# Performance work log

Hardware: AMD Instinct MI355X
Metric: run time of the kernel (lower is better)

The kernel has to match this reference:

```python
import jax, jax.numpy as jnp
import numpy as np

B, S, C, D, V = 64, 128, 32, 512, 20000

def setup_inputs() -> dict:
    key = jax.random.key(0)
    ks = jax.random.split(key, 16)
    sc = 1.0 / np.sqrt(D)
    emb = jax.random.normal(ks[0], (V + 1, D), jnp.float32) * 0.02
    emb = emb.at[V].set(0.0)  # padding_idx=-1 -> last row zero
    inp = dict(
        emb=emb,
        W_all_w=jax.random.uniform(ks[1], (4 * D, D), jnp.float32, -sc, sc),
        W_all_b=jnp.zeros((4 * D,), jnp.float32),
        U_all_w=jax.random.uniform(ks[2], (4 * D, D), jnp.float32, -sc, sc),
        U_all_b=jnp.zeros((4 * D,), jnp.float32),
        W_d_w=jax.random.uniform(ks[3], (D, D), jnp.float32, -sc, sc),
        W_d_b=jnp.zeros((D,), jnp.float32),
        sel_w=jax.random.uniform(ks[4], (64, 1), jnp.float32, -1.0, 1.0),
        sel_b=jnp.zeros((64,), jnp.float32),
        time_w=jax.random.uniform(ks[5], (D, 64), jnp.float32, -0.125, 0.125),
        time_b=jnp.zeros((D,), jnp.float32),
        out_w=jax.random.uniform(ks[6], (2, D), jnp.float32, -sc, sc),
        out_b=jnp.zeros((2,), jnp.float32),
        seq_time_step=jax.random.uniform(ks[7], (B, S), jnp.float32, 0.0, 365.0),
        input_seqs=jax.random.randint(ks[8], (B, S, C), 0, V),
        mask=jnp.zeros((B, S), bool),
        lengths=jax.random.randint(ks[9], (B,), 1, S),
        codemask=jnp.zeros((B, S, C), bool),
        label=jax.random.randint(ks[10], (B,), 0, 2),
    )
    return inp


def reference(emb, W_all_w, W_all_b, U_all_w, U_all_b, W_d_w, W_d_b,
              sel_w, sel_b, time_w, time_b, out_w, out_b, seq_time_step,
              input_seqs, mask, lengths, codemask, label):
    # visit embedding: sum code embeddings -> [B,S,D]
    x = emb[input_seqs].sum(axis=2)
    # time feature: 1 - tanh(selection_layer(t/180)^2) -> time_layer -> [B,S,D]
    t = (seq_time_step / 180.0)[..., None]                      # [B,S,1]
    tf = 1.0 - jnp.tanh(jnp.square(t * sel_w[:, 0] + sel_b))    # [B,S,64]
    tf = jnp.einsum('bsk,dk->bsd', tf, time_w) + time_b         # [B,S,D]
    # precompute input projection for all steps: [B,S,4D]
    ux = jnp.einsum('bsd,ed->bse', x, U_all_w) + U_all_b

    def step(carry, inputs):
        h, c = carry
        tf_s, ux_s = inputs                                      # [B,D], [B,4D]
        c_s1 = jnp.tanh(c @ W_d_w.T + W_d_b)
        c_adj = c - c_s1 + c_s1 * tf_s
        outs = h @ W_all_w.T + W_all_b + ux_s
        f, i, o, c_tmp = jnp.split(jax.nn.sigmoid(outs), 4, axis=1)
        c_new = f * c_adj + i * c_tmp
        h_new = o * jnp.tanh(c_new)
        return (h_new, c_new), h_new

    h0 = jnp.zeros((B, D), x.dtype)
    c0 = jnp.zeros((B, D), x.dtype)
    tf_t = jnp.swapaxes(tf, 0, 1)   # [S,B,D]
    ux_t = jnp.swapaxes(ux, 0, 1)   # [S,B,4D]
    _, hs = jax.lax.scan(step, (h0, c0), (tf_t, ux_t))
    outputs = jnp.swapaxes(hs, 0, 1)           # [B,S,D]
    pooled = outputs.max(axis=1)                # MaxPoolLayer without mask
    out = pooled @ out_w.T + out_b              # [B,2]
    return out
```

## Files before the change

### kernel.cpp

```cpp
#include <hip/hip_runtime.h>
#include <hip/hip_bf16.h>

#define B_ 64
#define S_ 128
#define C_ 32
#define D_ 512
#define V_ 20000

typedef float     f32x4  __attribute__((ext_vector_type(4)));
typedef _Float16  f16x8  __attribute__((ext_vector_type(8)));

#define OFF_XH   0ull
#define OFF_UH   8388608ull
#define OFF_AW   10485760ull
#define OFF_CB   13631488ull
#define OFF_SYNC 13639680ull
#define OFF_TWT  13647872ull
#define OFF_EMBH 13778944ull
#define OFF_TF   34259968ull
#define OFF_UX   42648576ull
#define OFF_XB2  76203008ull

#define SENT32 0x7FFF7FFFu

__global__ void k_zero(int4* __restrict__ p)
{
    p[blockIdx.x * 256 + threadIdx.x] = int4{0, 0, 0, 0};
}

__global__ void k_fill(int4* __restrict__ p)
{
    p[blockIdx.x * 256 + threadIdx.x] =
        int4{(int)SENT32, (int)SENT32, (int)SENT32, (int)SENT32};
}

__global__ void k_prep_wswz(const float* __restrict__ Wall, const float* __restrict__ Wd,
                            int4* __restrict__ AW)
{
    int i = blockIdx.x * 256 + threadIdx.x;
    int lane = i & 63;  int r = i >> 6;
    int kt = r & 15;    r >>= 4;
    int tile = r % 3;   r /= 3;
    int w = r & 7;      int m = r >> 3;
    int row16 = lane & 15, quad = lane >> 4;
    int q = tile * 2 + (row16 >> 3);
    int d = m * 64 + w * 8 + (row16 & 7);
    int k0 = kt * 32 + quad * 8;
    union { _Float16 h[8]; int4 v; } u;
    const float* src = nullptr;
    if (q < 4)       src = Wall + (size_t)(q * 512 + d) * 512 + k0;
    else if (q == 4) src = Wd   + (size_t)d * 512 + k0;
    #pragma unroll
    for (int j = 0; j < 8; j++) u.h[j] = src ? (_Float16)src[j] : (_Float16)0.f;
    AW[i] = u.v;
}

__global__ void k_prep_u(const float* __restrict__ U, _Float16* __restrict__ o)
{
    int i = blockIdx.x * 256 + threadIdx.x;
    o[i] = (_Float16)U[i];
}

__global__ void k_prep_cb(const float* __restrict__ a, const float* __restrict__ b,
                          float* __restrict__ o)
{
    int i = blockIdx.x * 256 + threadIdx.x;
    o[i] = a[i] + b[i];
}

__global__ void k_prep_emb(const float* __restrict__ e, _Float16* __restrict__ o)
{
    int i = blockIdx.x * 256 + threadIdx.x;
    float2 v = ((const float2*)e)[i];
    unsigned short hx = __builtin_bit_cast(unsigned short, (_Float16)v.x);
    unsigned short hy = __builtin_bit_cast(unsigned short, (_Float16)v.y);
    ((unsigned*)o)[i] = (unsigned)hx | ((unsigned)hy << 16);
}

__global__ void k_prep_twt(const float* __restrict__ tw, float* __restrict__ o)
{
    int i = blockIdx.x * 256 + threadIdx.x;
    int d = i >> 6, j = i & 63;
    o[j * 512 + d] = tw[i];
}

__global__ void k_embed2(const _Float16* __restrict__ embh, const int* __restrict__ seqs,
                         _Float16* __restrict__ xh)
{
    int bs = blockIdx.x;
    int t  = threadIdx.x;
    __shared__ int rows[32];
    if (t < 32) {
        int r = seqs[(size_t)bs * C_ + t];
        rows[t] = (r < 0) ? V_ : r;
    }
    __syncthreads();
    float ax = 0.f, ay = 0.f;
    #pragma unroll 4
    for (int c = 0; c < C_; c++) {
        unsigned v = *(const unsigned*)(embh + (size_t)rows[c] * D_ + 2 * t);
        ax += (float)__builtin_bit_cast(_Float16, (unsigned short)v);
        ay += (float)__builtin_bit_cast(_Float16, (unsigned short)(v >> 16));
    }
    unsigned short hx = __builtin_bit_cast(unsigned short, (_Float16)ax);
    unsigned short hy = __builtin_bit_cast(unsigned short, (_Float16)ay);
    *(unsigned*)(xh + (size_t)bs * D_ + 2 * t) = (unsigned)hx | ((unsigned)hy << 16);
}

__global__ __launch_bounds__(512) void k_tf2(
    const float* __restrict__ stime, const float* __restrict__ selw,
    const float* __restrict__ selb, const float* __restrict__ twT,
    const float* __restrict__ timeb, _Float16* __restrict__ tf)
{
    int bb = blockIdx.x;
    int t  = threadIdx.x;
    __shared__ float s1[16][64];
    for (int idx = t; idx < 1024; idx += 512) {
        int bl = idx >> 6, j = idx & 63;
        float tv = stime[bb * 16 + bl] * (1.0f / 180.0f);
        float u  = tv * selw[j] + selb[j];
        s1[bl][j] = 1.0f - tanhf(u * u);
    }
    __syncthreads();
    int d = t;
    float acc[16];
    float tb = timeb[d];
    #pragma unroll
    for (int l = 0; l < 16; l++) acc[l] = tb;
    for (int j = 0; j < 64; j++) {
        float wj = twT[j * 512 + d];
        #pragma unroll
        for (int l = 0; l < 16; l++) acc[l] = fmaf(s1[l][j], wj, acc[l]);
    }
    #pragma unroll
    for (int l = 0; l < 16; l++)
        tf[(size_t)(bb * 16 + l) * 512 + d] = (_Float16)acc[l];
}

__global__ __launch_bounds__(512) void k_gemm(const _Float16* __restrict__ A,
                                              const _Float16* __restrict__ Bm,
                                              _Float16* __restrict__ Cg)
{
    int lane = threadIdx.x & 63;
    int w    = threadIdx.x >> 6;
    int wm = w & 3, wn = w >> 2;
    int q = lane >> 4, r = lane & 15;
    int m0 = blockIdx.y * 128 + wm * 32;
    int n0 = blockIdx.x * 128 + wn * 64;

    const _Float16* pa0 = A  + (size_t)(m0 + r) * 512 + q * 8;
    const _Float16* pa1 = pa0 + (size_t)16 * 512;
    const _Float16* pb  = Bm + (size_t)(n0 + r) * 512 + q * 8;

    f32x4 acc[2][4] = {};
    for (int k = 0; k < 512; k += 32) {
        f16x8 a0 = *(const f16x8*)(pa0 + k);
        f16x8 a1 = *(const f16x8*)(pa1 + k);
        f16x8 b0 = *(const f16x8*)(pb + k);
        f16x8 b1 = *(const f16x8*)(pb + (size_t)16 * 512 + k);
        f16x8 b2 = *(const f16x8*)(pb + (size_t)32 * 512 + k);
        f16x8 b3 = *(const f16x8*)(pb + (size_t)48 * 512 + k);
        acc[0][0] = __builtin_amdgcn_mfma_f32_16x16x32_f16(a0, b0, acc[0][0], 0, 0, 0);
        acc[0][1] = __builtin_amdgcn_mfma_f32_16x16x32_f16(a0, b1, acc[0][1], 0, 0, 0);
        acc[0][2] = __builtin_amdgcn_mfma_f32_16x16x32_f16(a0, b2, acc[0][2], 0, 0, 0);
        acc[0][3] = __builtin_amdgcn_mfma_f32_16x16x32_f16(a0, b3, acc[0][3], 0, 0, 0);
        acc[1][0] = __builtin_amdgcn_mfma_f32_16x16x32_f16(a1, b0, acc[1][0], 0, 0, 0);
        acc[1][1] = __builtin_amdgcn_mfma_f32_16x16x32_f16(a1, b1, acc[1][1], 0, 0, 0);
        acc[1][2] = __builtin_amdgcn_mfma_f32_16x16x32_f16(a1, b2, acc[1][2], 0, 0, 0);
        acc[1][3] = __builtin_amdgcn_mfma_f32_16x16x32_f16(a1, b3, acc[1][3], 0, 0, 0);
    }
    for (int am = 0; am < 2; am++)
        for (int bn = 0; bn < 4; bn++) {
            int row = m0 + am * 16 + q * 4;
            int col = n0 + bn * 16 + r;
            _Float16* cp = Cg + (size_t)row * 2048 + col;
            #pragma unroll
            for (int t = 0; t < 4; t++) cp[(size_t)t * 2048] = (_Float16)acc[am][bn][t];
        }
}

__device__ __forceinline__ float fsigm(float x)
{
    return __builtin_amdgcn_rcpf(1.f + __expf(-x));
}
__device__ __forceinline__ float ftanh(float x)
{
    return 1.f - 2.f * __builtin_amdgcn_rcpf(1.f + __expf(2.f * x));
}

__global__ __launch_bounds__(512, 2) void k_rnn7(
    const int4* __restrict__ AW,
    const float* __restrict__ cbv, const float* __restrict__ wdb,
    const _Float16* __restrict__ ux, const _Float16* __restrict__ tf,
    const float* __restrict__ outw,
    float* __restrict__ pooled_red,
    unsigned long long* __restrict__ xb64)
{
    const int t    = threadIdx.x;
    const int gid  = blockIdx.x >> 3;
    const int m    = blockIdx.x & 7;
    const int b0   = gid * 2;
    const int w    = t >> 6;
    const int lane = t & 63;
    const int col  = lane & 15;
    const int quad = lane >> 4;

    int4 Af[48];
    {
        const int4* src = AW + (size_t)(m * 8 + w) * 3072;
        #pragma unroll
        for (int i = 0; i < 48; i++) Af[i] = src[i * 64 + lane];
    }

    __shared__ __align__(16) _Float16 xstg[4 * 544];
    __shared__ __align__(16) float cmat[8][4][48];
    __shared__ float pstg[2][64];

    const bool act = (lane < 16);
    const int  pb  = lane >> 3;
    const int  pj  = lane & 7;
    const int  dl  = w * 8 + pj;
    const int  d   = m * 64 + dl;

    float cbf = 0, cbi = 0, cbo = 0, cbc = 0, bdv = 0;
    if (act) {
        cbf = cbv[d]; cbi = cbv[512 + d]; cbo = cbv[1024 + d]; cbc = cbv[1536 + d];
        bdv = wdb[d];
    }
    float c_reg = 0.f, pool = -1e30f;
    const int dw = w * 64 + lane;

    for (int s = 0; s < S_; s++) {
        float uf = 0, ui = 0, uo = 0, uc = 0, tv = 0;
        if (act) {
            size_t bs = (size_t)(b0 + pb) * S_ + s;
            const _Float16* up = ux + bs * 2048 + d;
            uf = (float)up[0];    ui = (float)up[512];
            uo = (float)up[1024]; uc = (float)up[1536];
            tv = (float)tf[bs * 512 + d];
        }

        unsigned long long val = 0ull;
        if (s > 0) {
            const unsigned long long* src =
                xb64 + (((size_t)s * 32 + gid) * 8 + w) * 64 + lane;
            int tries = 0;
            for (;;) {
                val = __hip_atomic_load(src, __ATOMIC_RELAXED,
                                        __HIP_MEMORY_SCOPE_AGENT);
                if ((unsigned)val != SENT32 && (unsigned)(val >> 32) != SENT32)
                    break;
                if (++tries > (1 << 22)) break;
            }
        }
        __syncthreads();
        xstg[0 * 544 + dw] = __builtin_bit_cast(_Float16, (unsigned short)(val));
        xstg[2 * 544 + dw] = __builtin_bit_cast(_Float16, (unsigned short)(val >> 16));
        xstg[1 * 544 + dw] = __builtin_bit_cast(_Float16, (unsigned short)(val >> 32));
        xstg[3 * 544 + dw] = __builtin_bit_cast(_Float16, (unsigned short)(val >> 48));
        __syncthreads();

        f32x4 a0 = {0, 0, 0, 0}, a1 = {0, 0, 0, 0}, a2 = {0, 0, 0, 0};
        #pragma unroll
        for (int kt = 0; kt < 16; kt++) {
            f16x8 b = {};
            if (col < 4)
                b = *(const f16x8*)(xstg + col * 544 + kt * 32 + quad * 8);
            a0 = __builtin_amdgcn_mfma_f32_16x16x32_f16(
                     __builtin_bit_cast(f16x8, Af[kt]),      b, a0, 0, 0, 0);
            a1 = __builtin_amdgcn_mfma_f32_16x16x32_f16(
                     __builtin_bit_cast(f16x8, Af[16 + kt]), b, a1, 0, 0, 0);
            a2 = __builtin_amdgcn_mfma_f32_16x16x32_f16(
                     __builtin_bit_cast(f16x8, Af[32 + kt]), b, a2, 0, 0, 0);
        }

        if (col < 4) {
            *(f32x4*)&cmat[w][col][ 0 + quad * 4] = a0;
            *(f32x4*)&cmat[w][col][16 + quad * 4] = a1;
            *(f32x4*)&cmat[w][col][32 + quad * 4] = a2;
        }

        if (act) {
            float f_  = cmat[w][pb][ 0 + pj];
            float i_  = cmat[w][pb][ 8 + pj];
            float o_  = cmat[w][pb][16 + pj];
            float g_  = cmat[w][pb][24 + pj];
            float wd_ = cmat[w][2 + pb][32 + pj];
            float gf = fsigm(f_ + cbf + uf);
            float gi = fsigm(i_ + cbi + ui);
            float go = fsigm(o_ + cbo + uo);
            float gc = fsigm(g_ + cbc + uc);
            float cs1  = ftanh(wd_ + bdv);
            float cadj = c_reg - cs1 + cs1 * tv;
            float cn   = gf * cadj + gi * gc;
            float hn   = go * ftanh(cn);
            c_reg = cn;
            pool  = fmaxf(pool, hn);
            unsigned hh = __builtin_bit_cast(unsigned short, (_Float16)hn);
            unsigned cc = __builtin_bit_cast(unsigned short, (_Float16)cn);
            unsigned pk = hh | (cc << 16);
            unsigned other = __shfl(pk, lane + 8);
            if (pb == 0 && s != S_ - 1) {
                unsigned long long ov =
                    (unsigned long long)pk | ((unsigned long long)other << 32);
                unsigned long long* dst =
                    xb64 + (((size_t)(s + 1) * 32 + gid) * 8 + m) * 64 + dl;
                __hip_atomic_store(dst, ov, __ATOMIC_RELAXED,
                                   __HIP_MEMORY_SCOPE_AGENT);
            }
        }
    }

    if (act) pstg[pb][dl] = pool;
    __syncthreads();
    if (t < 128) {
        int b = t >> 6, l = t & 63;
        float pv = pstg[b][l];
        int dg = m * 64 + l;
        float p0 = pv * outw[dg], p1 = pv * outw[512 + dg];
        #pragma unroll
        for (int off = 32; off > 0; off >>= 1) {
            p0 += __shfl_down(p0, off);
            p1 += __shfl_down(p1, off);
        }
        if (l == 0) {
            atomicAdd(&pooled_red[2 * (b0 + b)],     p0);
            atomicAdd(&pooled_red[2 * (b0 + b) + 1], p1);
        }
    }
}

__global__ void k_out(const float* __restrict__ pr, const float* __restrict__ outb,
                      float* __restrict__ out)
{
    int i = threadIdx.x;
    if (i < 128) out[i] = pr[i] + outb[i & 1];
}

extern "C" void kernel_launch(void* const* d_in, const int* in_sizes, int n_in,
                              void* d_out, int out_size, void* d_ws, size_t ws_size,
                              hipStream_t stream)
{
    const float* emb   = (const float*)d_in[0];
    const float* Wall  = (const float*)d_in[1];
    const float* Wallb = (const float*)d_in[2];
    const float* Uall  = (const float*)d_in[3];
    const float* Uallb = (const float*)d_in[4];
    const float* Wdw   = (const float*)d_in[5];
    const float* Wdb   = (const float*)d_in[6];
    const float* selw  = (const float*)d_in[7];
    const float* selb  = (const float*)d_in[8];
    const float* timew = (const float*)d_in[9];
    const float* timeb = (const float*)d_in[10];
    const float* outw  = (const float*)d_in[11];
    const float* outb  = (const float*)d_in[12];
    const float* stime = (const float*)d_in[13];
    const int*   seqs  = (const int*)d_in[14];
    float* out = (float*)d_out;
    char*  ws  = (char*)d_ws;

    _Float16* xh   = (_Float16*)(ws + OFF_XH);
    _Float16* uh   = (_Float16*)(ws + OFF_UH);
    int4*     aw   = (int4*)(ws + OFF_AW);
    float*    cbp  = (float*)(ws + OFF_CB);
    float*    pred = (float*)(ws + OFF_SYNC + 4096);
    float*    twt  = (float*)(ws + OFF_TWT);
    _Float16* eh   = (_Float16*)(ws + OFF_EMBH);
    _Float16* tfp  = (_Float16*)(ws + OFF_TF);
    _Float16* uxp  = (_Float16*)(ws + OFF_UX);
    unsigned long long* xb = (unsigned long long*)(ws + OFF_XB2);

    k_zero     <<<2,     256, 0, stream>>>((int4*)(ws + OFF_SYNC));
    k_fill     <<<4096,  256, 0, stream>>>((int4*)(ws + OFF_XB2));
    k_prep_emb <<<20001, 256, 0, stream>>>(emb, eh);
    k_prep_wswz<<<768,   256, 0, stream>>>(Wall, Wdw, aw);
    k_prep_u   <<<4096,  256, 0, stream>>>(Uall, uh);
    k_prep_cb  <<<8,     256, 0, stream>>>(Wallb, Uallb, cbp);
    k_prep_twt <<<128,   256, 0, stream>>>(timew, twt);
    k_embed2   <<<B_ * S_, 256, 0, stream>>>(eh, seqs, xh);
    k_tf2      <<<512,   512, 0, stream>>>(stime, selw, selb, twt, timeb, tfp);
    k_gemm     <<<dim3(16, 64), 512, 0, stream>>>(xh, uh, uxp);
    k_rnn7     <<<256,   512, 0, stream>>>(aw, cbp, Wdb, uxp, tfp, outw, pred, xb);
    k_out      <<<1,     128, 0, stream>>>(pred, outb, out);
}
```

Measured before the change: 554.1 us.

## Fuse prep kernels into one launch and tile the input GEMM through LDS

Seven small preprocessing kernels (sentinel fill, bias add, transposes, fp16 conversions, weight swizzle) become one kernel that dispatches on block index. The final output kernel is removed: the output is seeded with the bias and the RNN atomically adds into it directly. The input-projection GEMM is rewritten to stage 128x64 tiles of A and B into LDS with an XOR swizzle via global_load_lds, giving each wave a 64x64 output tile to increase reuse over the direct-from-global version. The intent is to cut launch overhead and GEMM memory traffic, at the cost of more LDS use and two barriers per k-step.

```diff
diff --git a/kernel.cpp b/kernel.cpp
--- a/kernel.cpp
+++ b/kernel.cpp
@@ -10,11 +10,14 @@
 typedef float     f32x4  __attribute__((ext_vector_type(4)));
 typedef _Float16  f16x8  __attribute__((ext_vector_type(8)));
 
+#define AS1 __attribute__((address_space(1)))
+#define AS3 __attribute__((address_space(3)))
+
 #define OFF_XH   0ull
 #define OFF_UH   8388608ull
 #define OFF_AW   10485760ull
 #define OFF_CB   13631488ull
-#define OFF_SYNC 13639680ull
+#define OFF_PAD  13639680ull
 #define OFF_TWT  13647872ull
 #define OFF_EMBH 13778944ull
 #define OFF_TF   34259968ull
@@ -23,65 +26,68 @@
 
 #define SENT32 0x7FFF7FFFu
 
-__global__ void k_zero(int4* __restrict__ p)
-{
-    p[blockIdx.x * 256 + threadIdx.x] = int4{0, 0, 0, 0};
-}
-
-__global__ void k_fill(int4* __restrict__ p)
-{
-    p[blockIdx.x * 256 + threadIdx.x] =
-        int4{(int)SENT32, (int)SENT32, (int)SENT32, (int)SENT32};
-}
-
-__global__ void k_prep_wswz(const float* __restrict__ Wall, const float* __restrict__ Wd,
-                            int4* __restrict__ AW)
-{
-    int i = blockIdx.x * 256 + threadIdx.x;
-    int lane = i & 63;  int r = i >> 6;
-    int kt = r & 15;    r >>= 4;
-    int tile = r % 3;   r /= 3;
-    int w = r & 7;      int m = r >> 3;
-    int row16 = lane & 15, quad = lane >> 4;
-    int q = tile * 2 + (row16 >> 3);
-    int d = m * 64 + w * 8 + (row16 & 7);
-    int k0 = kt * 32 + quad * 8;
-    union { _Float16 h[8]; int4 v; } u;
-    const float* src = nullptr;
-    if (q < 4)       src = Wall + (size_t)(q * 512 + d) * 512 + k0;
-    else if (q == 4) src = Wd   + (size_t)d * 512 + k0;
-    #pragma unroll
-    for (int j = 0; j < 8; j++) u.h[j] = src ? (_Float16)src[j] : (_Float16)0.f;
-    AW[i] = u.v;
-}
-
-__global__ void k_prep_u(const float* __restrict__ U, _Float16* __restrict__ o)
-{
-    int i = blockIdx.x * 256 + threadIdx.x;
-    o[i] = (_Float16)U[i];
-}
-
-__global__ void k_prep_cb(const float* __restrict__ a, const float* __restrict__ b,
-                          float* __restrict__ o)
-{
-    int i = blockIdx.x * 256 + threadIdx.x;
-    o[i] = a[i] + b[i];
-}
-
-__global__ void k_prep_emb(const float* __restrict__ e, _Float16* __restrict__ o)
-{
-    int i = blockIdx.x * 256 + threadIdx.x;
-    float2 v = ((const float2*)e)[i];
-    unsigned short hx = __builtin_bit_cast(unsigned short, (_Float16)v.x);
-    unsigned short hy = __builtin_bit_cast(unsigned short, (_Float16)v.y);
-    ((unsigned*)o)[i] = (unsigned)hx | ((unsigned)hy << 16);
-}
-
-__global__ void k_prep_twt(const float* __restrict__ tw, float* __restrict__ o)
-{
-    int i = blockIdx.x * 256 + threadIdx.x;
-    int d = i >> 6, j = i & 63;
-    o[j * 512 + d] = tw[i];
+__global__ void k_prep_fused(
+    const float* __restrict__ outb, float* __restrict__ outv,
+    int4* __restrict__ fillp,
+    const float* __restrict__ Wallb, const float* __restrict__ Uallb,
+    float* __restrict__ cb,
+    const float* __restrict__ tw, float* __restrict__ twt,
+    const float* __restrict__ U, _Float16* __restrict__ uh,
+    const float* __restrict__ Wall, const float* __restrict__ Wd,
+    int4* __restrict__ AW,
+    const float* __restrict__ emb, _Float16* __restrict__ eh)
+{
+    const int blk = blockIdx.x;
+    const int t   = threadIdx.x;
+    if (blk < 1) {
+        if (t < 128) outv[t] = outb[t & 1];
+    } else if (blk < 4097) {
+        fillp[(blk - 1) * 256 + t] =
+            int4{(int)SENT32, (int)SENT32, (int)SENT32, (int)SENT32};
+    } else if (blk < 4098) {
+        #pragma unroll
+        for (int k = 0; k < 8; k++) {
+            int i = t * 8 + k;
+            cb[i] = Wallb[i] + Uallb[i];
+        }
+    } else if (blk < 4130) {
+        int i2 = (blk - 4098) * 256 + t;
+        #pragma unroll
+        for (int k = 0; k < 4; k++) {
+            int i = i2 * 4 + k;
+            twt[(i & 63) * 512 + (i >> 6)] = tw[i];
+        }
+    } else if (blk < 5154) {
+        int i = (blk - 4130) * 256 + t;
+        float4 v = ((const float4*)U)[i];
+        union { _Float16 h[4]; unsigned long long u; } pk;
+        pk.h[0] = (_Float16)v.x; pk.h[1] = (_Float16)v.y;
+        pk.h[2] = (_Float16)v.z; pk.h[3] = (_Float16)v.w;
+        ((unsigned long long*)uh)[i] = pk.u;
+    } else if (blk < 5922) {
+        int i = (blk - 5154) * 256 + t;
+        int lane = i & 63;  int r = i >> 6;
+        int kt = r & 15;    r >>= 4;
+        int tile = r % 3;   r /= 3;
+        int w = r & 7;      int m = r >> 3;
+        int row16 = lane & 15, quad = lane >> 4;
+        int q = tile * 2 + (row16 >> 3);
+        int d = m * 64 + w * 8 + (row16 & 7);
+        int k0 = kt * 32 + quad * 8;
+        union { _Float16 h[8]; int4 v; } u;
+        const float* src = nullptr;
+        if (q < 4)       src = Wall + (size_t)(q * 512 + d) * 512 + k0;
+        else if (q == 4) src = Wd   + (size_t)d * 512 + k0;
+        #pragma unroll
+        for (int j = 0; j < 8; j++) u.h[j] = src ? (_Float16)src[j] : (_Float16)0.f;
+        AW[i] = u.v;
+    } else {
+        int i = (blk - 5922) * 256 + t;
+        float2 v = ((const float2*)emb)[i];
+        unsigned short hx = __builtin_bit_cast(unsigned short, (_Float16)v.x);
+        unsigned short hy = __builtin_bit_cast(unsigned short, (_Float16)v.y);
+        ((unsigned*)eh)[i] = (unsigned)hx | ((unsigned)hy << 16);
+    }
 }
 
 __global__ void k_embed2(const _Float16* __restrict__ embh, const int* __restrict__ seqs,
@@ -137,45 +143,70 @@
         tf[(size_t)(bb * 16 + l) * 512 + d] = (_Float16)acc[l];
 }
 
-__global__ __launch_bounds__(512) void k_gemm(const _Float16* __restrict__ A,
-                                              const _Float16* __restrict__ Bm,
-                                              _Float16* __restrict__ Cg)
-{
-    int lane = threadIdx.x & 63;
-    int w    = threadIdx.x >> 6;
-    int wm = w & 3, wn = w >> 2;
-    int q = lane >> 4, r = lane & 15;
-    int m0 = blockIdx.y * 128 + wm * 32;
-    int n0 = blockIdx.x * 128 + wn * 64;
-
-    const _Float16* pa0 = A  + (size_t)(m0 + r) * 512 + q * 8;
-    const _Float16* pa1 = pa0 + (size_t)16 * 512;
-    const _Float16* pb  = Bm + (size_t)(n0 + r) * 512 + q * 8;
-
-    f32x4 acc[2][4] = {};
-    for (int k = 0; k < 512; k += 32) {
-        f16x8 a0 = *(const f16x8*)(pa0 + k);
-        f16x8 a1 = *(const f16x8*)(pa1 + k);
-        f16x8 b0 = *(const f16x8*)(pb + k);
-        f16x8 b1 = *(const f16x8*)(pb + (size_t)16 * 512 + k);
-        f16x8 b2 = *(const f16x8*)(pb + (size_t)32 * 512 + k);
-        f16x8 b3 = *(const f16x8*)(pb + (size_t)48 * 512 + k);
-        acc[0][0] = __builtin_amdgcn_mfma_f32_16x16x32_f16(a0, b0, acc[0][0], 0, 0, 0);
-        acc[0][1] = __builtin_amdgcn_mfma_f32_16x16x32_f16(a0, b1, acc[0][1], 0, 0, 0);
-        acc[0][2] = __builtin_amdgcn_mfma_f32_16x16x32_f16(a0, b2, acc[0][2], 0, 0, 0);
-        acc[0][3] = __builtin_amdgcn_mfma_f32_16x16x32_f16(a0, b3, acc[0][3], 0, 0, 0);
-        acc[1][0] = __builtin_amdgcn_mfma_f32_16x16x32_f16(a1, b0, acc[1][0], 0, 0, 0);
-        acc[1][1] = __builtin_amdgcn_mfma_f32_16x16x32_f16(a1, b1, acc[1][1], 0, 0, 0);
-        acc[1][2] = __builtin_amdgcn_mfma_f32_16x16x32_f16(a1, b2, acc[1][2], 0, 0, 0);
-        acc[1][3] = __builtin_amdgcn_mfma_f32_16x16x32_f16(a1, b3, acc[1][3], 0, 0, 0);
-    }
-    for (int am = 0; am < 2; am++)
-        for (int bn = 0; bn < 4; bn++) {
-            int row = m0 + am * 16 + q * 4;
-            int col = n0 + bn * 16 + r;
+__device__ __forceinline__ void stage16(const _Float16* g, _Float16* l)
+{
+#if __has_builtin(__builtin_amdgcn_global_load_lds)
+    __builtin_amdgcn_global_load_lds((const AS1 void*)g, (AS3 void*)l, 16, 0, 0);
+#else
+    *(int4*)l = *(const int4*)g;
+#endif
+}
+
+__global__ __launch_bounds__(256, 4) void k_gemm3(const _Float16* __restrict__ A,
+                                                  const _Float16* __restrict__ Bm,
+                                                  _Float16* __restrict__ Cg)
+{
+    __shared__ __align__(16) _Float16 As[128 * 64];
+    __shared__ __align__(16) _Float16 Bs[128 * 64];
+    const int t = threadIdx.x;
+    const int w = t >> 6, lane = t & 63;
+    const int wm = w & 1, wn = w >> 1;
+    const int m0 = blockIdx.y * 128, n0 = blockIdx.x * 128;
+    const int r16 = lane & 15, quad = lane >> 4;
+
+    const int srow = w * 8 + (lane >> 3);
+    const int k8g  = (lane & 7) ^ ((lane >> 3) & 7);
+    const _Float16* ga = A  + (size_t)(m0 + srow) * 512 + k8g * 8;
+    const _Float16* gb = Bm + (size_t)(n0 + srow) * 512 + k8g * 8;
+    _Float16* la = As + srow * 64 + (lane & 7) * 8;
+    _Float16* lb = Bs + srow * 64 + (lane & 7) * 8;
+
+    f32x4 acc[4][4] = {};
+    for (int k0 = 0; k0 < 512; k0 += 64) {
+        __syncthreads();
+        #pragma unroll
+        for (int r = 0; r < 4; r++) {
+            stage16(ga + k0 + (size_t)r * 32 * 512, la + r * 32 * 64);
+            stage16(gb + k0 + (size_t)r * 32 * 512, lb + r * 32 * 64);
+        }
+        __syncthreads();
+        #pragma unroll
+        for (int sub = 0; sub < 2; sub++) {
+            f16x8 af[4], bf[4];
+            const int ksl = ((sub * 4 + quad) ^ (r16 & 7)) * 8;
+            #pragma unroll
+            for (int i = 0; i < 4; i++) {
+                af[i] = *(const f16x8*)(As + (wm * 64 + i * 16 + r16) * 64 + ksl);
+                bf[i] = *(const f16x8*)(Bs + (wn * 64 + i * 16 + r16) * 64 + ksl);
+            }
+            #pragma unroll
+            for (int i = 0; i < 4; i++)
+                #pragma unroll
+                for (int j = 0; j < 4; j++)
+                    acc[i][j] = __builtin_amdgcn_mfma_f32_16x16x32_f16(
+                                    af[i], bf[j], acc[i][j], 0, 0, 0);
+        }
+    }
+    #pragma unroll
+    for (int i = 0; i < 4; i++)
+        #pragma unroll
+        for (int j = 0; j < 4; j++) {
+            int row = m0 + wm * 64 + i * 16 + quad * 4;
+            int col = n0 + wn * 64 + j * 16 + r16;
             _Float16* cp = Cg + (size_t)row * 2048 + col;
             #pragma unroll
-            for (int t = 0; t < 4; t++) cp[(size_t)t * 2048] = (_Float16)acc[am][bn][t];
+            for (int rg = 0; rg < 4; rg++)
+                cp[(size_t)rg * 2048] = (_Float16)acc[i][j][rg];
         }
 }
 
@@ -193,7 +224,7 @@
     const float* __restrict__ cbv, const float* __restrict__ wdb,
     const _Float16* __restrict__ ux, const _Float16* __restrict__ tf,
     const float* __restrict__ outw,
-    float* __restrict__ pooled_red,
+    float* __restrict__ out,
     unsigned long long* __restrict__ xb64)
 {
     const int t    = threadIdx.x;
@@ -324,17 +355,10 @@
             p1 += __shfl_down(p1, off);
         }
         if (l == 0) {
-            atomicAdd(&pooled_red[2 * (b0 + b)],     p0);
-            atomicAdd(&pooled_red[2 * (b0 + b) + 1], p1);
-        }
-    }
-}
-
-__global__ void k_out(const float* __restrict__ pr, const float* __restrict__ outb,
-                      float* __restrict__ out)
-{
-    int i = threadIdx.x;
-    if (i < 128) out[i] = pr[i] + outb[i & 1];
+            atomicAdd(&out[2 * (b0 + b)],     p0);
+            atomicAdd(&out[2 * (b0 + b) + 1], p1);
+        }
+    }
 }
 
 extern "C" void kernel_launch(void* const* d_in, const int* in_sizes, int n_in,
@@ -363,23 +387,21 @@
     _Float16* uh   = (_Float16*)(ws + OFF_UH);
     int4*     aw   = (int4*)(ws + OFF_AW);
     float*    cbp  = (float*)(ws + OFF_CB);
-    float*    pred = (float*)(ws + OFF_SYNC + 4096);
     float*    twt  = (float*)(ws + OFF_TWT);
     _Float16* eh   = (_Float16*)(ws + OFF_EMBH);
     _Float16* tfp  = (_Float16*)(ws + OFF_TF);
     _Float16* uxp  = (_Float16*)(ws + OFF_UX);
     unsigned long long* xb = (unsigned long long*)(ws + OFF_XB2);
 
-    k_zero     <<<2,     256, 0, stream>>>((int4*)(ws + OFF_SYNC));
-    k_fill     <<<4096,  256, 0, stream>>>((int4*)(ws + OFF_XB2));
-    k_prep_emb <<<20001, 256, 0, stream>>>(emb, eh);
-    k_prep_wswz<<<768,   256, 0, stream>>>(Wall, Wdw, aw);
-    k_prep_u   <<<4096,  256, 0, stream>>>(Uall, uh);
-    k_prep_cb  <<<8,     256, 0, stream>>>(Wallb, Uallb, cbp);
-    k_prep_twt <<<128,   256, 0, stream>>>(timew, twt);
-    k_embed2   <<<B_ * S_, 256, 0, stream>>>(eh, seqs, xh);
-    k_tf2      <<<512,   512, 0, stream>>>(stime, selw, selb, twt, timeb, tfp);
-    k_gemm     <<<dim3(16, 64), 512, 0, stream>>>(xh, uh, uxp);
-    k_rnn7     <<<256,   512, 0, stream>>>(aw, cbp, Wdb, uxp, tfp, outw, pred, xb);
-    k_out      <<<1,     128, 0, stream>>>(pred, outb, out);
-}
+    k_prep_fused<<<25923, 256, 0, stream>>>(
+        outb, out, (int4*)(ws + OFF_XB2),
+        Wallb, Uallb, cbp,
+        timew, twt,
+        Uall, uh,
+        Wall, Wdw, aw,
+        emb, eh);
+    k_embed2 <<<B_ * S_, 256, 0, stream>>>(eh, seqs, xh);
+    k_tf2    <<<512,     512, 0, stream>>>(stime, selw, selb, twt, timeb, tfp);
+    k_gemm3  <<<dim3(16, 64), 256, 0, stream>>>(xh, uh, uxp);
+    k_rnn7   <<<256,     512, 0, stream>>>(aw, cbp, Wdb, uxp, tfp, outw, out, xb);
+}
```

New measurement: 471.1 us. 15.0% less time.
